# Kernel optimization log

Measured on AMD Instinct MI355X. Metric: run time of the kernel, lower is better.

## Reference

```python
import jax, jax.numpy as jnp
import numpy as np

B, NPER, F, D, E, NUM_STEPS = 256, 512, 256, 32, 524288, 4
N = B * NPER
INIT_TAU, TAU_SCALE, STEP_ALPHA = 0.1, 0.5, 5.0


def setup_inputs() -> dict:
    key = jax.random.key(0)
    ks = jax.random.split(key, 10)
    x_start = jax.random.uniform(ks[0], (N,), jnp.float32, 0.1, 1.0)   # strictly positive iterate
    x_solution = jax.random.uniform(ks[1], (N,), jnp.float32, 0.0, 1.0)
    q = jax.random.normal(ks[2], (N,), jnp.float32)
    edge_src = jax.random.randint(ks[3], (E,), 0, N, jnp.int32)
    edge_dst = jax.random.randint(ks[4], (E,), 0, N, jnp.int32)
    vals_batch = jnp.repeat(jnp.arange(B, dtype=jnp.int32), NPER)      # equal-sized graphs
    proj_matrix = jax.random.normal(ks[5], (B, NPER, F), jnp.float32) / np.float32(np.sqrt(NPER))
    W_in = jax.random.normal(ks[6], (2, D), jnp.float32) / np.float32(np.sqrt(2.0))
    b_in = jnp.zeros((D,), jnp.float32)
    W_msg = jax.random.normal(ks[7], (D, D), jnp.float32) / np.float32(np.sqrt(D))
    b_msg = jnp.zeros((D,), jnp.float32)
    W_out = jax.random.normal(ks[8], (D, 1), jnp.float32) / np.float32(np.sqrt(D))
    b_out = jnp.zeros((1,), jnp.float32)
    return {"x_start": x_start, "x_solution": x_solution, "q": q,
            "proj_matrix": proj_matrix, "W_in": W_in, "b_in": b_in,
            "W_msg": W_msg, "b_msg": b_msg, "W_out": W_out, "b_out": b_out,
            "edge_src": edge_src, "edge_dst": edge_dst, "vals_batch": vals_batch}


def _l1_normalize(x, batch):
    # per-graph L1 normalization: x / sum_i |x_i| over the graph segment
    s = jax.ops.segment_sum(jnp.abs(x), batch, num_segments=B)
    return x / (s[batch] + 1e-12)


def _line_search(x, d, batch, max_alpha):
    # largest per-graph alpha s.t. x + alpha*d >= 0, capped at max_alpha
    ratio = jnp.where(d < 0, x / jnp.maximum(-d, 1e-12), max_alpha)
    a = jnp.clip(jax.ops.segment_min(ratio, batch, num_segments=B), 0.0, max_alpha)
    return a[batch]  # gathered back to per-node


def _gnn(xs, q, edge_src, edge_dst, W_in, b_in, W_msg, b_msg, W_out, b_out):
    h = jax.nn.relu(jnp.stack([xs, q], axis=-1) @ W_in + b_in)      # [N, D]
    m = h[edge_src] @ W_msg + b_msg                                  # [E, D]
    agg = jax.ops.segment_sum(m, edge_dst, num_segments=N)          # [N, D]
    h2 = jax.nn.relu(h + agg)
    return h2 @ W_out[:, 0] + b_out[0]                               # [N]


def reference(x_start, x_solution, q, proj_matrix, W_in, b_in, W_msg, b_msg,
              W_out, b_out, edge_src, edge_dst, vals_batch):
    tau = INIT_TAU
    xs = x_start
    preds, labels = [], []
    for _ in range(NUM_STEPS):
        pred = _gnn(xs, q, edge_src, edge_dst, W_in, b_in, W_msg, b_msg, W_out, b_out)
        preds.append(pred)
        labels.append(_l1_normalize(x_solution - xs, vals_batch))
        p = _l1_normalize(jax.lax.stop_gradient(pred), vals_batch)   # .detach() in torch
        direction = p + 3.0 * tau / (xs + tau)
        tau = max(tau * TAU_SCALE, 1e-5)
        # to_dense_batch with equal graph sizes == reshape; project onto nullspace basis
        dd = direction.reshape(B, NPER)
        df = jnp.einsum('bnf,bn->bf', proj_matrix, dd)               # [B, F]
        pproj = jnp.einsum('bnf,bf->bn', proj_matrix, df).reshape(-1)  # [N]
        alpha = _line_search(xs, pproj, vals_batch, STEP_ALPHA) * 0.995
        xs = xs + alpha * pproj
    return jnp.stack(preds, axis=1), jnp.stack(labels, axis=1)       # each [N, NUM_STEPS]
```

## Files before the change

kernel.cpp:

```cpp
#include <hip/hip_runtime.h>

#define BB 256
#define NPER 512
#define FF 256
#define DD 32
#define EE 524288
#define NN (BB*NPER)
#define NSTEPS 4

__device__ __forceinline__ float bflo(unsigned u) { return __uint_as_float(u << 16); }
__device__ __forceinline__ float bfhi(unsigned u) { return __uint_as_float(u & 0xFFFF0000u); }
__device__ __forceinline__ unsigned rtn_bf16(unsigned u) {
    return (u + 0x7FFFu + ((u >> 16) & 1u)) >> 16;
}


__global__ void k_degpack(const int* __restrict__ dst, unsigned* __restrict__ deg,
                          const float* __restrict__ xs0, const float* __restrict__ q,
                          float2* __restrict__ xq) {
    int t = blockIdx.x * blockDim.x + threadIdx.x;
    if (t < NN) { float2 v; v.x = xs0[t]; v.y = q[t]; xq[t] = v; }
    atomicAdd(&deg[dst[t]], 1u);
}

__global__ void k_bsum(const unsigned* __restrict__ deg, unsigned* __restrict__ bsum) {
    __shared__ unsigned r[256];
    int t = threadIdx.x;
    r[t] = deg[blockIdx.x * 256 + t];
    __syncthreads();
    for (int o = 128; o > 0; o >>= 1) { if (t < o) r[t] += r[t + o]; __syncthreads(); }
    if (t == 0) bsum[blockIdx.x] = r[0];
}

__global__ void k_scanb(const unsigned* __restrict__ bsum, unsigned* __restrict__ bbase) {
    __shared__ unsigned r[512];
    int t = threadIdx.x;
    unsigned own = bsum[t];
    r[t] = own;
    __syncthreads();
    for (int o = 1; o < 512; o <<= 1) {
        unsigned v = (t >= o) ? r[t - o] : 0u;
        __syncthreads();
        r[t] += v;
        __syncthreads();
    }
    bbase[t] = r[t] - own;
}

__global__ void k_offsets(const unsigned* __restrict__ deg, const unsigned* __restrict__ bbase,
                          unsigned* __restrict__ rowstart, unsigned* __restrict__ cursor) {
    __shared__ unsigned r[256];
    int t = threadIdx.x;
    int i = blockIdx.x * 256 + t;
    unsigned d = deg[i];
    r[t] = d;
    __syncthreads();
    for (int o = 1; o < 256; o <<= 1) {
        unsigned v = (t >= o) ? r[t - o] : 0u;
        __syncthreads();
        r[t] += v;
        __syncthreads();
    }
    unsigned excl = r[t] - d + bbase[blockIdx.x];
    rowstart[i] = excl;
    cursor[i] = excl;
}

__global__ void k_fill(const int* __restrict__ src, const int* __restrict__ dst,
                       unsigned* __restrict__ cursor, int* __restrict__ csr_src) {
    int e = blockIdx.x * blockDim.x + threadIdx.x;
    unsigned pos = atomicAdd(&cursor[dst[e]], 1u);
    csr_src[pos] = src[e];
}


__global__ void k_node_g(const float2* __restrict__ xq,
                         const float* __restrict__ Win, const float* __restrict__ bin,
                         const unsigned* __restrict__ rowstart, const unsigned* __restrict__ deg,
                         const int* __restrict__ csr_src,
                         const float* __restrict__ Wmsg, const float* __restrict__ bmsg,
                         const float* __restrict__ Wout, const float* __restrict__ bout,
                         float* __restrict__ pred, float* __restrict__ out_preds, int step) {
    int tid = threadIdx.x;
    int d = tid & 31;
    int i = blockIdx.x * 8 + (tid >> 5);
    float w0 = Win[d], w1 = Win[DD + d], b0 = bin[d];
    float wcol[DD];
    #pragma unroll
    for (int k = 0; k < DD; ++k) wcol[k] = Wmsg[k * DD + d];
    unsigned rs = rowstart[i];
    unsigned dg = deg[i];
    unsigned nfull = dg < 32u ? dg : 32u;
    float xv = 0.f, qv = 0.f;
    if ((unsigned)d < nfull) {
        int sv = csr_src[rs + d];
        float2 v = xq[sv];
        xv = v.x; qv = v.y;
    }
    float s = 0.f;
    for (unsigned j = 0; j < nfull; ++j) {
        float xj = __shfl(xv, (int)j, 32);
        float qj = __shfl(qv, (int)j, 32);
        s += fmaxf(xj * w0 + qj * w1 + b0, 0.f);
    }
    for (unsigned j = 32; j < dg; ++j) {
        int sv = csr_src[rs + j];
        float2 v = xq[sv];
        s += fmaxf(v.x * w0 + v.y * w1 + b0, 0.f);
    }
    float2 self = xq[i];
    float hval = fmaxf(self.x * w0 + self.y * w1 + b0, 0.f);
    float agg = (float)dg * bmsg[d];
    #pragma unroll
    for (int k = 0; k < DD; ++k) agg += __shfl(s, k, 32) * wcol[k];
    float h2 = fmaxf(hval + agg, 0.f);
    float v = h2 * Wout[d];
    for (int o = 16; o > 0; o >>= 1) v += __shfl_down(v, o, 32);
    if (d == 0) {
        float pr = v + bout[0];
        pred[i] = pr;
        out_preds[i * NSTEPS + step] = pr;
    }
}

__global__ __launch_bounds__(512) void k_step(const float* __restrict__ Pf,
                                              unsigned short* __restrict__ Pbf,
                                              float2* __restrict__ xq,
                                              const float* __restrict__ xsol,
                                              const float* __restrict__ pred,
                                              float* __restrict__ out_labels,
                                              float tau, int step) {
    __shared__ float ddl[NPER];
    __shared__ float sl[8 * FF];
    __shared__ float dfl[FF];
    __shared__ float pp[NPER];
    __shared__ float red[8], red2[8];
    int b = blockIdx.x;
    int t = threadIdx.x;
    int w = t >> 6, lane = t & 63;
    int i = b * NPER + t;
    float x = xq[i].x;
    float r = xsol[i] - x;
    float p = pred[i];
    float a1 = fabsf(r), a2 = fabsf(p);
    #pragma unroll
    for (int o = 32; o > 0; o >>= 1) {
        a1 += __shfl_down(a1, o, 64);
        a2 += __shfl_down(a2, o, 64);
    }
    if (lane == 0) { red[w] = a1; red2[w] = a2; }
    __syncthreads();
    float Sr = 1e-12f, Sp = 1e-12f;
    #pragma unroll
    for (int k = 0; k < 8; ++k) { Sr += red[k]; Sp += red2[k]; }
    out_labels[i * NSTEPS + step] = r / Sr;
    if (step == NSTEPS - 1) return;
    ddl[t] = p / Sp + 3.0f * tau / (x + tau);
    __syncthreads();

    float4 acc = {0.f, 0.f, 0.f, 0.f};
    size_t rowbase = (size_t)(b * NPER + w * 64) * FF;
    if (step == 0) {
        const float4* Pr = (const float4*)(Pf + rowbase) + lane;
        uint2* Pw = (uint2*)(Pbf + rowbase) + lane;
        #pragma unroll 4
        for (int n = 0; n < 64; ++n) {
            float4 pv = Pr[(size_t)n * 64];
            float sc = ddl[w * 64 + n];
            acc.x += pv.x * sc; acc.y += pv.y * sc;
            acc.z += pv.z * sc; acc.w += pv.w * sc;
            unsigned u0 = rtn_bf16(__float_as_uint(pv.x));
            unsigned u1 = rtn_bf16(__float_as_uint(pv.y));
            unsigned u2 = rtn_bf16(__float_as_uint(pv.z));
            unsigned u3 = rtn_bf16(__float_as_uint(pv.w));
            uint2 o; o.x = u0 | (u1 << 16); o.y = u2 | (u3 << 16);
            Pw[(size_t)n * 64] = o;
        }
    } else {
        const uint2* Pr = (const uint2*)(Pbf + rowbase) + lane;
        #pragma unroll 8
        for (int n = 0; n < 64; ++n) {
            uint2 pv = Pr[(size_t)n * 64];
            float sc = ddl[w * 64 + n];
            acc.x += bflo(pv.x) * sc; acc.y += bfhi(pv.x) * sc;
            acc.z += bflo(pv.y) * sc; acc.w += bfhi(pv.y) * sc;
        }
    }
    ((float4*)sl)[w * 64 + lane] = acc;
    __syncthreads();
    if (t < FF) {
        float v = 0.f;
        #pragma unroll
        for (int k = 0; k < 8; ++k) v += sl[k * FF + t];
        dfl[t] = v;
    }
    __syncthreads();

    int g = t >> 5, l5 = t & 31;
    float4 dfa = ((const float4*)dfl)[l5 * 2];
    float4 dfb = ((const float4*)dfl)[l5 * 2 + 1];
    const uint4* Pr4 = (const uint4*)(Pbf + (size_t)(b * NPER + g * 32) * FF) + l5;
    #pragma unroll 4
    for (int it = 0; it < 32; ++it) {
        uint4 pv = Pr4[(size_t)it * 32];
        float a = bflo(pv.x) * dfa.x + bfhi(pv.x) * dfa.y
                + bflo(pv.y) * dfa.z + bfhi(pv.y) * dfa.w
                + bflo(pv.z) * dfb.x + bfhi(pv.z) * dfb.y
                + bflo(pv.w) * dfb.z + bfhi(pv.w) * dfb.w;
        #pragma unroll
        for (int o = 16; o > 0; o >>= 1) a += __shfl_down(a, o, 32);
        if (l5 == 0) pp[g * 32 + it] = a;
    }
    __syncthreads();

    float d = pp[t];
    float ratio = (d < 0.f) ? (x / fmaxf(-d, 1e-12f)) : 5.0f;
    float m = ratio;
    #pragma unroll
    for (int o = 32; o > 0; o >>= 1) m = fminf(m, __shfl_down(m, o, 64));
    if (lane == 0) red[w] = m;
    __syncthreads();
    float mm = red[0];
    #pragma unroll
    for (int k = 1; k < 8; ++k) mm = fminf(mm, red[k]);
    float alpha = fminf(fmaxf(mm, 0.f), 5.0f) * 0.995f;
    xq[i].x = x + alpha * d;
}


extern "C" void kernel_launch(void* const* d_in, const int* in_sizes, int n_in,
                              void* d_out, int out_size, void* d_ws, size_t ws_size,
                              hipStream_t stream) {
    const float* x_start = (const float*)d_in[0];
    const float* x_sol   = (const float*)d_in[1];
    const float* q       = (const float*)d_in[2];
    const float* P       = (const float*)d_in[3];
    const float* Win     = (const float*)d_in[4];
    const float* bin     = (const float*)d_in[5];
    const float* Wmsg    = (const float*)d_in[6];
    const float* bmsg    = (const float*)d_in[7];
    const float* Wout    = (const float*)d_in[8];
    const float* bout    = (const float*)d_in[9];
    const int*   esrc    = (const int*)d_in[10];
    const int*   edst    = (const int*)d_in[11];

    float* out_preds  = (float*)d_out;
    float* out_labels = (float*)d_out + (size_t)NN * NSTEPS;

    float* w = (float*)d_ws;
    float2* xq  = (float2*)w; w += 2 * (size_t)NN;
    float* pred  = w; w += NN;
    unsigned* deg      = (unsigned*)w; w += NN;
    unsigned* rowstart = (unsigned*)w; w += NN;
    unsigned* cursor   = (unsigned*)w; w += NN;
    unsigned* bsum     = (unsigned*)w; w += NN / 256;
    unsigned* bbase    = (unsigned*)w; w += NN / 256;
    int* csr_src       = (int*)w;      w += EE;
    unsigned short* Pbf = (unsigned short*)w;

    hipMemsetAsync(deg, 0, NN * sizeof(unsigned), stream);
    k_degpack<<<EE / 256, 256, 0, stream>>>(edst, deg, x_start, q, xq);
    k_bsum<<<NN / 256, 256, 0, stream>>>(deg, bsum);
    k_scanb<<<1, NN / 256, 0, stream>>>(bsum, bbase);
    k_offsets<<<NN / 256, 256, 0, stream>>>(deg, bbase, rowstart, cursor);
    k_fill<<<EE / 256, 256, 0, stream>>>(esrc, edst, cursor, csr_src);

    float tau = 0.1f;
    for (int step = 0; step < NSTEPS; ++step) {
        k_node_g<<<NN / 8, 256, 0, stream>>>(xq, Win, bin, rowstart, deg, csr_src,
                                             Wmsg, bmsg, Wout, bout, pred, out_preds, step);
        k_step<<<BB, 512, 0, stream>>>(P, Pbf, xq, x_sol, pred, out_labels, tau, step);
        tau = fmaxf(tau * 0.5f, 1e-5f);
    }
}
```

Before: 514.2 us.

## Split per-graph projection step into multi-block kernels with atomic reductions

Replaces the single 256-block step kernel, one block per graph, with several kernels. The L1 sums move into the GNN kernel through atomics, the P^T·d product is split four ways per graph with atomicAdd into df, the P·df projection runs on 2048 blocks with an atomicMin line search, and a separate update kernel applies the step. The goal is better occupancy on the bandwidth-bound projection passes, which previously used only 256 blocks on a many-CU GPU. In exchange it adds extra kernel launches, ping-pong scratch buffers and float atomic ordering nondeterminism.

```diff
diff --git a/kernel.cpp b/kernel.cpp
--- a/kernel.cpp
+++ b/kernel.cpp
@@ -73,17 +73,32 @@
     csr_src[pos] = src[e];
 }
 
-
-__global__ void k_node_g(const float2* __restrict__ xq,
+__global__ void k_init(float* __restrict__ df0, float* __restrict__ accs0,
+                       unsigned* __restrict__ alpha0) {
+    int t = threadIdx.x;
+    df0[blockIdx.x * 256 + t] = 0.f;
+    if (t == 0) {
+        accs0[blockIdx.x] = 0.f;
+        accs0[BB + blockIdx.x] = 0.f;
+        alpha0[blockIdx.x] = 0x7f800000u;
+    }
+}
+
+
+__global__ void k_node_g(const float2* __restrict__ xq, const float* __restrict__ xsol,
                          const float* __restrict__ Win, const float* __restrict__ bin,
                          const unsigned* __restrict__ rowstart, const unsigned* __restrict__ deg,
                          const int* __restrict__ csr_src,
                          const float* __restrict__ Wmsg, const float* __restrict__ bmsg,
                          const float* __restrict__ Wout, const float* __restrict__ bout,
-                         float* __restrict__ pred, float* __restrict__ out_preds, int step) {
+                         float* __restrict__ pred, float* __restrict__ out_preds,
+                         float* __restrict__ accsP, int step) {
+    __shared__ float sp_[8], sr_[8];
     int tid = threadIdx.x;
     int d = tid & 31;
-    int i = blockIdx.x * 8 + (tid >> 5);
+    int ni = tid >> 5;
+    int i = blockIdx.x * 8 + ni;
+    int b = blockIdx.x >> 6;
     float w0 = Win[d], w1 = Win[DD + d], b0 = bin[d];
     float wcol[DD];
     #pragma unroll
@@ -120,53 +135,49 @@
         float pr = v + bout[0];
         pred[i] = pr;
         out_preds[i * NSTEPS + step] = pr;
-    }
-}
-
-__global__ __launch_bounds__(512) void k_step(const float* __restrict__ Pf,
-                                              unsigned short* __restrict__ Pbf,
-                                              float2* __restrict__ xq,
-                                              const float* __restrict__ xsol,
-                                              const float* __restrict__ pred,
-                                              float* __restrict__ out_labels,
-                                              float tau, int step) {
-    __shared__ float ddl[NPER];
-    __shared__ float sl[8 * FF];
-    __shared__ float dfl[FF];
-    __shared__ float pp[NPER];
-    __shared__ float red[8], red2[8];
-    int b = blockIdx.x;
-    int t = threadIdx.x;
-    int w = t >> 6, lane = t & 63;
-    int i = b * NPER + t;
-    float x = xq[i].x;
-    float r = xsol[i] - x;
-    float p = pred[i];
-    float a1 = fabsf(r), a2 = fabsf(p);
-    #pragma unroll
-    for (int o = 32; o > 0; o >>= 1) {
-        a1 += __shfl_down(a1, o, 64);
-        a2 += __shfl_down(a2, o, 64);
-    }
-    if (lane == 0) { red[w] = a1; red2[w] = a2; }
-    __syncthreads();
-    float Sr = 1e-12f, Sp = 1e-12f;
-    #pragma unroll
-    for (int k = 0; k < 8; ++k) { Sr += red[k]; Sp += red2[k]; }
-    out_labels[i * NSTEPS + step] = r / Sr;
-    if (step == NSTEPS - 1) return;
-    ddl[t] = p / Sp + 3.0f * tau / (x + tau);
-    __syncthreads();
-
+        sp_[ni] = fabsf(pr);
+        sr_[ni] = fabsf(xsol[i] - self.x);
+    }
+    __syncthreads();
+    if (tid == 0) {
+        float a = 0.f, c = 0.f;
+        #pragma unroll
+        for (int k = 0; k < 8; ++k) { a += sp_[k]; c += sr_[k]; }
+        atomicAdd(&accsP[b], c);
+        atomicAdd(&accsP[BB + b], a);
+    }
+}
+
+__global__ void k_df(const float* __restrict__ Pf, unsigned short* __restrict__ Pbf,
+                     const float2* __restrict__ xq, const float* __restrict__ xsol,
+                     const float* __restrict__ pred, float* __restrict__ out_labels,
+                     const float* __restrict__ accsP, float* __restrict__ dfP,
+                     float tau, int step) {
+    __shared__ float ddl[128];
+    __shared__ float sl[4 * FF];
+    int b = blockIdx.x >> 2, sp = blockIdx.x & 3;
+    int t = threadIdx.x, w = t >> 6, lane = t & 63;
+    int nb = b * NPER + sp * 128;
+    float Sr = accsP[b] + 1e-12f;
+    float Sp = accsP[BB + b] + 1e-12f;
+    if (t < 128) {
+        int i = nb + t;
+        float x = xq[i].x;
+        float r = xsol[i] - x;
+        out_labels[i * NSTEPS + step] = r / Sr;
+        ddl[t] = pred[i] / Sp + 3.0f * tau / (x + tau);
+    }
+    __syncthreads();
     float4 acc = {0.f, 0.f, 0.f, 0.f};
-    size_t rowbase = (size_t)(b * NPER + w * 64) * FF;
+    size_t rowbase = (size_t)(nb + w * 32) * FF;
+    const float* dw = &ddl[w * 32];
     if (step == 0) {
         const float4* Pr = (const float4*)(Pf + rowbase) + lane;
         uint2* Pw = (uint2*)(Pbf + rowbase) + lane;
         #pragma unroll 4
-        for (int n = 0; n < 64; ++n) {
+        for (int n = 0; n < 32; ++n) {
             float4 pv = Pr[(size_t)n * 64];
-            float sc = ddl[w * 64 + n];
+            float sc = dw[n];
             acc.x += pv.x * sc; acc.y += pv.y * sc;
             acc.z += pv.z * sc; acc.w += pv.w * sc;
             unsigned u0 = rtn_bf16(__float_as_uint(pv.x));
@@ -179,52 +190,81 @@
     } else {
         const uint2* Pr = (const uint2*)(Pbf + rowbase) + lane;
         #pragma unroll 8
-        for (int n = 0; n < 64; ++n) {
+        for (int n = 0; n < 32; ++n) {
             uint2 pv = Pr[(size_t)n * 64];
-            float sc = ddl[w * 64 + n];
+            float sc = dw[n];
             acc.x += bflo(pv.x) * sc; acc.y += bfhi(pv.x) * sc;
             acc.z += bflo(pv.y) * sc; acc.w += bfhi(pv.y) * sc;
         }
     }
     ((float4*)sl)[w * 64 + lane] = acc;
     __syncthreads();
-    if (t < FF) {
-        float v = 0.f;
-        #pragma unroll
-        for (int k = 0; k < 8; ++k) v += sl[k * FF + t];
-        dfl[t] = v;
-    }
-    __syncthreads();
-
-    int g = t >> 5, l5 = t & 31;
+    float v = sl[t] + sl[FF + t] + sl[2 * FF + t] + sl[3 * FF + t];
+    atomicAdd(&dfP[b * FF + t], v);
+}
+
+__global__ void k_pproj(const unsigned short* __restrict__ Pbf, const float* __restrict__ dfP,
+                        const float2* __restrict__ xq,
+                        float* __restrict__ pproj, unsigned* __restrict__ alphaP) {
+    __shared__ float dfl[FF];
+    __shared__ float mred[8];
+    int t = threadIdx.x, g = t >> 5, l5 = t & 31;
+    int b = blockIdx.x >> 3;
+    dfl[t] = dfP[b * FF + t];
+    __syncthreads();
     float4 dfa = ((const float4*)dfl)[l5 * 2];
     float4 dfb = ((const float4*)dfl)[l5 * 2 + 1];
-    const uint4* Pr4 = (const uint4*)(Pbf + (size_t)(b * NPER + g * 32) * FF) + l5;
-    #pragma unroll 4
-    for (int it = 0; it < 32; ++it) {
-        uint4 pv = Pr4[(size_t)it * 32];
+    int n0 = blockIdx.x * 64 + g * 8;
+    float m = 5.0f;
+    #pragma unroll
+    for (int it = 0; it < 8; ++it) {
+        int n = n0 + it;
+        uint4 pv = ((const uint4*)(Pbf + (size_t)n * FF))[l5];
         float a = bflo(pv.x) * dfa.x + bfhi(pv.x) * dfa.y
                 + bflo(pv.y) * dfa.z + bfhi(pv.y) * dfa.w
                 + bflo(pv.z) * dfb.x + bfhi(pv.z) * dfb.y
                 + bflo(pv.w) * dfb.z + bfhi(pv.w) * dfb.w;
         #pragma unroll
         for (int o = 16; o > 0; o >>= 1) a += __shfl_down(a, o, 32);
-        if (l5 == 0) pp[g * 32 + it] = a;
-    }
-    __syncthreads();
-
-    float d = pp[t];
-    float ratio = (d < 0.f) ? (x / fmaxf(-d, 1e-12f)) : 5.0f;
-    float m = ratio;
-    #pragma unroll
-    for (int o = 32; o > 0; o >>= 1) m = fminf(m, __shfl_down(m, o, 64));
-    if (lane == 0) red[w] = m;
-    __syncthreads();
-    float mm = red[0];
-    #pragma unroll
-    for (int k = 1; k < 8; ++k) mm = fminf(mm, red[k]);
-    float alpha = fminf(fmaxf(mm, 0.f), 5.0f) * 0.995f;
-    xq[i].x = x + alpha * d;
+        if (l5 == 0) {
+            pproj[n] = a;
+            float x = xq[n].x;
+            float ratio = (a < 0.f) ? (x / fmaxf(-a, 1e-12f)) : 5.0f;
+            m = fminf(m, ratio);
+        }
+    }
+    if (l5 == 0) mred[g] = m;
+    __syncthreads();
+    if (t == 0) {
+        float mm = mred[0];
+        #pragma unroll
+        for (int k = 1; k < 8; ++k) mm = fminf(mm, mred[k]);
+        atomicMin(&alphaP[b], __float_as_uint(mm));
+    }
+}
+
+__global__ void k_upd(const unsigned* __restrict__ alphaP, const float* __restrict__ pproj,
+                      float2* __restrict__ xq,
+                      float* __restrict__ dfN, float* __restrict__ accsN,
+                      unsigned* __restrict__ alphaN) {
+    int t = threadIdx.x;
+    int i = blockIdx.x * 256 + t;
+    int b = i >> 9;
+    float a = __uint_as_float(alphaP[b]);
+    a = fminf(fmaxf(a, 0.f), 5.0f) * 0.995f;
+    xq[i].x += a * pproj[i];
+    if (t < 128) dfN[blockIdx.x * 128 + t] = 0.f;
+    else if (t == 128) accsN[blockIdx.x] = 0.f;
+    else if (t == 129 && blockIdx.x < BB) alphaN[blockIdx.x] = 0x7f800000u;
+}
+
+__global__ void k_labels(const float2* __restrict__ xq, const float* __restrict__ xsol,
+                         const float* __restrict__ accsP, float* __restrict__ out_labels,
+                         int step) {
+    int i = blockIdx.x * 256 + threadIdx.x;
+    int b = i >> 9;
+    float Sr = accsP[b] + 1e-12f;
+    out_labels[i * NSTEPS + step] = (xsol[i] - xq[i].x) / Sr;
 }
 
 
@@ -250,6 +290,10 @@
     float* w = (float*)d_ws;
     float2* xq  = (float2*)w; w += 2 * (size_t)NN;
     float* pred  = w; w += NN;
+    float* pproj = w; w += NN;
+    float* df2   = w; w += 2 * (size_t)BB * FF;
+    float* accs2 = w; w += 2 * 2 * BB;
+    unsigned* alpha2 = (unsigned*)w; w += 2 * BB;
     unsigned* deg      = (unsigned*)w; w += NN;
     unsigned* rowstart = (unsigned*)w; w += NN;
     unsigned* cursor   = (unsigned*)w; w += NN;
@@ -260,6 +304,7 @@
 
     hipMemsetAsync(deg, 0, NN * sizeof(unsigned), stream);
     k_degpack<<<EE / 256, 256, 0, stream>>>(edst, deg, x_start, q, xq);
+    k_init<<<BB, 256, 0, stream>>>(df2, accs2, alpha2);
     k_bsum<<<NN / 256, 256, 0, stream>>>(deg, bsum);
     k_scanb<<<1, NN / 256, 0, stream>>>(bsum, bbase);
     k_offsets<<<NN / 256, 256, 0, stream>>>(deg, bbase, rowstart, cursor);
@@ -267,9 +312,23 @@
 
     float tau = 0.1f;
     for (int step = 0; step < NSTEPS; ++step) {
-        k_node_g<<<NN / 8, 256, 0, stream>>>(xq, Win, bin, rowstart, deg, csr_src,
-                                             Wmsg, bmsg, Wout, bout, pred, out_preds, step);
-        k_step<<<BB, 512, 0, stream>>>(P, Pbf, xq, x_sol, pred, out_labels, tau, step);
+        int par = step & 1, np = par ^ 1;
+        float* accsP = accs2 + par * 2 * BB;
+        float* dfP   = df2 + (size_t)par * BB * FF;
+        unsigned* alphaP = alpha2 + par * BB;
+        k_node_g<<<NN / 8, 256, 0, stream>>>(xq, x_sol, Win, bin, rowstart, deg, csr_src,
+                                             Wmsg, bmsg, Wout, bout, pred, out_preds,
+                                             accsP, step);
+        if (step < NSTEPS - 1) {
+            k_df<<<BB * 4, 256, 0, stream>>>(P, Pbf, xq, x_sol, pred, out_labels,
+                                             accsP, dfP, tau, step);
+            k_pproj<<<NN / 64, 256, 0, stream>>>(Pbf, dfP, xq, pproj, alphaP);
+            k_upd<<<NN / 256, 256, 0, stream>>>(alphaP, pproj, xq,
+                                                df2 + (size_t)np * BB * FF,
+                                                accs2 + np * 2 * BB, alpha2 + np * BB);
+        } else {
+            k_labels<<<NN / 256, 256, 0, stream>>>(xq, x_sol, accsP, out_labels, step);
+        }
         tau = fmaxf(tau * 0.5f, 1e-5f);
     }
 }
```

New measurement: 658.8 us. 28.1% more time.
